# Performance work log

Hardware: AMD Instinct MI355X
Metric: run time of the kernel (lower is better)

Reference implementation:

```python
import jax, jax.numpy as jnp
import numpy as np

BETA_NORM = 1
ETA_THRESHOLD = 0.3
EPS = 1e-8


def setup_inputs() -> dict:
    key = jax.random.key(0)
    x = jax.random.normal(key, (4, 4096, 64), dtype=jnp.float32)
    return {"x": x}


def reference(x) -> jnp.ndarray:
    # x: (B, S, N) CSI input
    x_mag = jnp.abs(x)
    if BETA_NORM == 1:
        norms = jnp.sum(x_mag, axis=-1)                    # (B, S) L1 norm
    else:
        norms = jnp.sqrt(jnp.sum(x_mag * x_mag, axis=-1))  # (B, S) L2 norm

    B, S = norms.shape
    t = jnp.arange(S)[:, None]          # (S, 1)
    tau = jnp.arange(1, S)[None, :]     # (1, S-1) candidate lags
    j = t - tau                          # (S, S-1) index t - tau
    valid = j >= 0                       # tau <= t (triangular range)
    jc = jnp.clip(j, 0, S - 1)

    # norms[b, t - tau] gathered for all (t, tau): (B, S, S-1)
    past = norms[:, jc]
    eta_t = 1.0 - past / (norms[:, :, None] + EPS)
    crossed = valid[None, :, :] & (eta_t > ETA_THRESHOLD)

    # first (smallest) tau that crosses the threshold; 0 if none
    BIG = S  # sentinel larger than any valid tau
    tau_or_big = jnp.where(crossed, tau[None, :, :], BIG)  # (B, S, S-1)
    min_tau = jnp.min(tau_or_big, axis=-1)                 # (B, S)
    tc = jnp.where(min_tau < BIG, min_tau, 0).astype(jnp.float32)
    return tc
```

## Files before the change

kernel.cpp:

```cpp
#include <hip/hip_runtime.h>


#define SS 4096
typedef unsigned long long u64;

template <typename T>
__global__ void __launch_bounds__(1024)
tc_norms_kernel(const float4* __restrict__ x4, T* __restrict__ nrm,
                T* __restrict__ cmn)
{
    __shared__ T smin[16];
    int ci   = blockIdx.x;
    int wave = threadIdx.x >> 6;
    int lane = threadIdx.x & 63;
    int g    = lane >> 4;
    int e    = lane & 15;

    int row = (ci << 6) + (wave << 2) + g;
    float4 p = x4[row * 16 + e];
    T a = (T)fabsf(p.x) + (T)fabsf(p.y) + (T)fabsf(p.z) + (T)fabsf(p.w);
    #pragma unroll
    for (int off = 8; off > 0; off >>= 1)
        a += __shfl_xor(a, off, 64);
    if (e == 0) nrm[row] = a;

    T m = (e == 0) ? a : (T)1e300;
    {
        T o = __shfl_xor(m, 16, 64); m = (o < m) ? o : m;
        o   = __shfl_xor(m, 32, 64); m = (o < m) ? o : m;
    }
    if (lane == 0) smin[wave] = m;
    __syncthreads();
    if (threadIdx.x < 16) {
        T m2 = smin[threadIdx.x];
        #pragma unroll
        for (int off = 8; off > 0; off >>= 1) {
            T o = __shfl_xor(m2, off, 64);
            m2 = (o < m2) ? o : m2;
        }
        if (threadIdx.x == 0) cmn[ci] = m2;
    }
}

template <typename T>
__global__ void __launch_bounds__(1024)
tc_scan_kernel(const T* __restrict__ nrm, const T* __restrict__ cmn,
               float* __restrict__ out)
{
    __shared__ T sn[64];
    __shared__ T scm[64];
    int ci   = blockIdx.x;
    int b    = ci >> 6;
    int c    = ci & 63;
    int wave = threadIdx.x >> 6;
    int lane = threadIdx.x & 63;

    if (wave == 0)      sn[lane]  = nrm[(ci << 6) + lane];
    else if (wave == 1) scm[lane] = cmn[(b << 6) + lane];
    __syncthreads();

    T v  = sn[lane];
    T cm = scm[lane];
    float res[4];
    #pragma unroll
    for (int k = 0; k < 4; ++k) {
        int pos = (wave << 2) + k;
        T thr = (T)0.7 * (sn[pos] + (T)1e-8);
        int r = 0;
        u64 m = __ballot(lane < pos && v < thr);
        if (m) {
            r = pos - (63 - __clzll(m));
        } else {
            u64 mc = __ballot(lane < c && cm < thr);
            if (mc) {
                int cc = 63 - __clzll(mc);
                T v2 = nrm[(b << 12) + (cc << 6) + lane];
                u64 m2 = __ballot(v2 < thr);
                r = ((c - cc) << 6) + pos - (63 - __clzll(m2));
            }
        }
        res[k] = (float)r;
    }
    if (lane == 0)
        ((float4*)out)[ci * 16 + wave] =
            make_float4(res[0], res[1], res[2], res[3]);
}

extern "C" void kernel_launch(void* const* d_in, const int* in_sizes, int n_in,
                              void* d_out, int out_size, void* d_ws, size_t ws_size,
                              hipStream_t stream) {
    const float4* x4 = (const float4*)d_in[0];
    float* out = (float*)d_out;
    int nrows  = in_sizes[0] / 64;
    int nchunk = nrows / 64;

    if (ws_size >= (size_t)(nrows + nchunk) * sizeof(double)) {
        double* nrm = (double*)d_ws;
        double* cmn = nrm + nrows;
        tc_norms_kernel<double><<<nchunk, 1024, 0, stream>>>(x4, nrm, cmn);
        tc_scan_kernel<double><<<nchunk, 1024, 0, stream>>>(nrm, cmn, out);
    } else {
        float* nrm = (float*)d_ws;
        float* cmn = nrm + nrows;
        tc_norms_kernel<float><<<nchunk, 1024, 0, stream>>>(x4, nrm, cmn);
        tc_scan_kernel<float><<<nchunk, 1024, 0, stream>>>(nrm, cmn, out);
    }
}
```

Baseline: 56.78 us.

## Fuse norm and scan kernels into one launch with shared-memory norms

Merges the norm computation and the threshold scan into a single kernel. Each block handles one quarter of a batch row and recomputes norms for every prefix row it needs into shared memory, which removes the workspace round-trip and the second launch. The cost is redundant norm work across the four blocks of each batch, only 16 blocks in total (poor GPU occupancy), and a serial 64-position loop per wave in place of 4 positions.

```diff
diff --git a/kernel.cpp b/kernel.cpp
--- a/kernel.cpp
+++ b/kernel.cpp
@@ -4,105 +4,80 @@
 #define SS 4096
 typedef unsigned long long u64;
 
-template <typename T>
 __global__ void __launch_bounds__(1024)
-tc_norms_kernel(const float4* __restrict__ x4, T* __restrict__ nrm,
-                T* __restrict__ cmn)
+tc_fused_kernel(const float4* __restrict__ x4, float* __restrict__ out)
 {
-    __shared__ T smin[16];
-    int ci   = blockIdx.x;
-    int wave = threadIdx.x >> 6;
-    int lane = threadIdx.x & 63;
-    int g    = lane >> 4;
-    int e    = lane & 15;
+    __shared__ double sn[SS];
+    __shared__ double scm[64];
 
-    int row = (ci << 6) + (wave << 2) + g;
-    float4 p = x4[row * 16 + e];
-    T a = (T)fabsf(p.x) + (T)fabsf(p.y) + (T)fabsf(p.z) + (T)fabsf(p.w);
-    #pragma unroll
-    for (int off = 8; off > 0; off >>= 1)
-        a += __shfl_xor(a, off, 64);
-    if (e == 0) nrm[row] = a;
+    const int bi   = blockIdx.x;
+    const int b    = bi >> 2;
+    const int q    = bi & 3;
+    const int wave = threadIdx.x >> 6;
+    const int lane = threadIdx.x & 63;
+    const int g    = lane >> 4;
+    const int e    = lane & 15;
 
-    T m = (e == 0) ? a : (T)1e300;
-    {
-        T o = __shfl_xor(m, 16, 64); m = (o < m) ? o : m;
-        o   = __shfl_xor(m, 32, 64); m = (o < m) ? o : m;
+    const int R = (q + 1) * 16;
+    const float4* xb = x4 + (size_t)b * SS * 16;
+
+    #pragma unroll 8
+    for (int r = 0; r < R; ++r) {
+        int row = (r << 6) + (wave << 2) + g;
+        float4 p = xb[row * 16 + e];
+        double a = (double)fabsf(p.x) + (double)fabsf(p.y)
+                 + (double)fabsf(p.z) + (double)fabsf(p.w);
+        #pragma unroll
+        for (int off = 8; off > 0; off >>= 1)
+            a += __shfl_xor(a, off, 64);
+        if (e == 0) sn[row] = a;
     }
-    if (lane == 0) smin[wave] = m;
-    __syncthreads();
-    if (threadIdx.x < 16) {
-        T m2 = smin[threadIdx.x];
-        #pragma unroll
-        for (int off = 8; off > 0; off >>= 1) {
-            T o = __shfl_xor(m2, off, 64);
-            m2 = (o < m2) ? o : m2;
-        }
-        if (threadIdx.x == 0) cmn[ci] = m2;
-    }
-}
-
-template <typename T>
-__global__ void __launch_bounds__(1024)
-tc_scan_kernel(const T* __restrict__ nrm, const T* __restrict__ cmn,
-               float* __restrict__ out)
-{
-    __shared__ T sn[64];
-    __shared__ T scm[64];
-    int ci   = blockIdx.x;
-    int b    = ci >> 6;
-    int c    = ci & 63;
-    int wave = threadIdx.x >> 6;
-    int lane = threadIdx.x & 63;
-
-    if (wave == 0)      sn[lane]  = nrm[(ci << 6) + lane];
-    else if (wave == 1) scm[lane] = cmn[(b << 6) + lane];
     __syncthreads();
 
-    T v  = sn[lane];
-    T cm = scm[lane];
-    float res[4];
-    #pragma unroll
-    for (int k = 0; k < 4; ++k) {
-        int pos = (wave << 2) + k;
-        T thr = (T)0.7 * (sn[pos] + (T)1e-8);
-        int r = 0;
-        u64 m = __ballot(lane < pos && v < thr);
-        if (m) {
-            r = pos - (63 - __clzll(m));
-        } else {
-            u64 mc = __ballot(lane < c && cm < thr);
-            if (mc) {
-                int cc = 63 - __clzll(mc);
-                T v2 = nrm[(b << 12) + (cc << 6) + lane];
-                u64 m2 = __ballot(v2 < thr);
-                r = ((c - cc) << 6) + pos - (63 - __clzll(m2));
+    for (int c = wave; c < R; c += 16) {
+        double m = sn[(c << 6) + lane];
+        #pragma unroll
+        for (int off = 32; off > 0; off >>= 1) {
+            double o = __shfl_xor(m, off, 64);
+            m = (o < m) ? o : m;
+        }
+        if (lane == 0) scm[c] = m;
+    }
+    __syncthreads();
+
+    {
+        const int c = (q << 4) + wave;
+        const double v  = sn[(c << 6) + lane];
+        const double cm = (lane < c) ? scm[lane] : 1e300;
+        float myres = 0.f;
+        for (int pos = 0; pos < 64; ++pos) {
+            double thr = 0.7 * (__shfl(v, pos, 64) + 1e-8);
+            int r = 0;
+            u64 m = __ballot(lane < pos && v < thr);
+            if (m) {
+                r = pos - (63 - __clzll(m));
+            } else {
+                u64 mc = __ballot(cm < thr);
+                if (mc) {
+                    int cc = 63 - __clzll(mc);
+                    double v2 = sn[(cc << 6) + lane];
+                    u64 m2 = __ballot(v2 < thr);
+                    r = ((c - cc) << 6) + pos - (63 - __clzll(m2));
+                }
             }
+            if (lane == pos) myres = (float)r;
         }
-        res[k] = (float)r;
+        out[(b << 12) + (c << 6) + lane] = myres;
     }
-    if (lane == 0)
-        ((float4*)out)[ci * 16 + wave] =
-            make_float4(res[0], res[1], res[2], res[3]);
 }
 
 extern "C" void kernel_launch(void* const* d_in, const int* in_sizes, int n_in,
                               void* d_out, int out_size, void* d_ws, size_t ws_size,
                               hipStream_t stream) {
+    (void)d_ws; (void)ws_size; (void)n_in; (void)out_size;
     const float4* x4 = (const float4*)d_in[0];
     float* out = (float*)d_out;
-    int nrows  = in_sizes[0] / 64;
-    int nchunk = nrows / 64;
-
-    if (ws_size >= (size_t)(nrows + nchunk) * sizeof(double)) {
-        double* nrm = (double*)d_ws;
-        double* cmn = nrm + nrows;
-        tc_norms_kernel<double><<<nchunk, 1024, 0, stream>>>(x4, nrm, cmn);
-        tc_scan_kernel<double><<<nchunk, 1024, 0, stream>>>(nrm, cmn, out);
-    } else {
-        float* nrm = (float*)d_ws;
-        float* cmn = nrm + nrows;
-        tc_norms_kernel<float><<<nchunk, 1024, 0, stream>>>(x4, nrm, cmn);
-        tc_scan_kernel<float><<<nchunk, 1024, 0, stream>>>(nrm, cmn, out);
-    }
+    int nrows = in_sizes[0] / 64;
+    int nb    = nrows / SS;
+    tc_fused_kernel<<<nb * 4, 1024, 0, stream>>>(x4, out);
 }
```

Result: slower. 99.06 us (+74.5%).
